# Kernel optimization log

Hardware: AMD Instinct MI355X
Metric: run time of the kernel (lower is better)

Reference implementation:

```python
import jax, jax.numpy as jnp
import numpy as np

GAMMA = 0.3      # LinearSpike surrogate slope (Bellec et al. 2018)
TIMESTEPS = 8
DROPOUT = 0.2

@jax.custom_vjp
def spike_fn(mem_thr):
    # forward: Heaviside spike; backward: piecewise-linear surrogate
    return (mem_thr > 0).astype(mem_thr.dtype)

def _spike_fwd(m):
    return (m > 0).astype(m.dtype), m

def _spike_bwd(m, g):
    return (GAMMA * jnp.maximum(1.0 - jnp.abs(m), 0.0) * g,)

spike_fn.defvjp(_spike_fwd, _spike_bwd)

def conv(x, w, stride=1, pad=1):
    return jax.lax.conv_general_dilated(
        x, w, (stride, stride), [(pad, pad), (pad, pad)],
        dimension_numbers=('NCHW', 'OIHW', 'NCHW'))

def avgpool2(x):
    B, C, H, W = x.shape
    return x.reshape(B, C, H // 2, 2, W // 2, 2).mean(axis=(3, 5))

def lif(mem, delta, leak, thr):
    mem = leak * mem + delta                  # leaky integrate
    mem_thr = mem / thr - 1.0                 # normalized membrane
    out = spike_fn(mem_thr)                   # binary spike
    mem = mem - thr * (mem_thr > 0).astype(mem.dtype)  # soft reset
    return mem, out

def setup_inputs() -> dict:
    key = jax.random.key(0)
    ks = jax.random.split(key, 24)
    B = 32
    def w(k, o, i, kh):
        std = float(np.sqrt(2.0 / (kh * kh * o)))  # matches _initialize_weights2
        return jax.random.normal(k, (o, i, kh, kh), jnp.float32) * std
    def mask(k, shape):
        keep = jax.random.bernoulli(k, 1.0 - DROPOUT, shape)
        return keep.astype(jnp.float32) / (1.0 - DROPOUT)
    return {
        'x': jax.random.normal(ks[0], (B, 3, 32, 32), jnp.float32),
        'w_pre0': w(ks[1], 64, 3, 3),
        'w_pre1': w(ks[2], 64, 64, 3),
        'w_pre2': w(ks[3], 64, 64, 3),
        'w1a': w(ks[4], 64, 64, 3),  'w1b': w(ks[5], 64, 64, 3),
        'w2a': w(ks[6], 128, 64, 3), 'w2b': w(ks[7], 128, 128, 3), 'w2i': w(ks[8], 128, 64, 1),
        'w3a': w(ks[9], 256, 128, 3), 'w3b': w(ks[10], 256, 256, 3), 'w3i': w(ks[11], 256, 128, 1),
        'w4a': w(ks[12], 512, 256, 3), 'w4b': w(ks[13], 512, 512, 3), 'w4i': w(ks[14], 512, 256, 1),
        'w_fc': jax.random.normal(ks[15], (10, 512 * 2 * 2), jnp.float32) * 0.01,
        'thr': jnp.ones((11,), jnp.float32),
        'leak': jnp.ones((11,), jnp.float32),
        'mask2': mask(ks[16], (B, 64, 32, 32)),
        'mask5': mask(ks[17], (B, 64, 32, 32)),
        'mask9': mask(ks[18], (B, 64, 16, 16)),
        'mask11': mask(ks[19], (B, 128, 8, 8)),
        'mask13': mask(ks[20], (B, 256, 4, 4)),
        'mask15': mask(ks[21], (B, 512, 2, 2)),
    }

def _forward(x, w_pre0, w_pre1, w_pre2, w1a, w1b, w2a, w2b, w2i,
             w3a, w3b, w3i, w4a, w4b, w4i, w_fc, thr, leak,
             mask2, mask5, mask9, mask11, mask13, mask15):
    B = x.shape[0]
    f32 = jnp.float32
    mems0 = (
        jnp.zeros((B, 64, 32, 32), f32), jnp.zeros((B, 64, 32, 32), f32),
        jnp.zeros((B, 64, 32, 32), f32),
        jnp.zeros((B, 64, 16, 16), f32), jnp.zeros((B, 64, 16, 16), f32),
        jnp.zeros((B, 128, 8, 8), f32), jnp.zeros((B, 128, 8, 8), f32),
        jnp.zeros((B, 256, 4, 4), f32), jnp.zeros((B, 256, 4, 4), f32),
        jnp.zeros((B, 512, 2, 2), f32), jnp.zeros((B, 512, 2, 2), f32),
        jnp.zeros((B, 10), f32),  # output accumulator mem
    )

    def step(carry, _):
        m0, m1, m2, m3, m4, m5, m6, m7, m8, m9, m10, mfc = carry
        # pre_process: (conv->spike->dropout) x2, conv->spike, avgpool2
        m0, o = lif(m0, conv(x, w_pre0), leak[0], thr[0]); o = o * mask2
        m1, o = lif(m1, conv(o, w_pre1), leak[1], thr[1]); o = o * mask5
        m2, o = lif(m2, conv(o, w_pre2), leak[2], thr[2])
        o = avgpool2(o)  # 32x32 -> 16x16
        # layer1 BasicBlock (stride 1, identity shortcut)
        inp = o
        m3, o = lif(m3, conv(inp, w1a), leak[3], thr[3]); o = o * mask9
        m4, o = lif(m4, conv(o, w1b) + inp, leak[4], thr[4])
        # layer2 BasicBlock (stride 2, 1x1 conv shortcut)
        inp = o
        m5, o = lif(m5, conv(inp, w2a, stride=2), leak[5], thr[5]); o = o * mask11
        m6, o = lif(m6, conv(o, w2b) + conv(inp, w2i, stride=2, pad=0), leak[6], thr[6])
        # layer3
        inp = o
        m7, o = lif(m7, conv(inp, w3a, stride=2), leak[7], thr[7]); o = o * mask13
        m8, o = lif(m8, conv(o, w3b) + conv(inp, w3i, stride=2, pad=0), leak[8], thr[8])
        # layer4
        inp = o
        m9, o = lif(m9, conv(inp, w4a, stride=2), leak[9], thr[9]); o = o * mask15
        m10, o = lif(m10, conv(o, w4b) + conv(inp, w4i, stride=2, pad=0), leak[10], thr[10])
        # output layer: pure accumulation of classifier current over timesteps
        mfc = mfc + o.reshape(B, -1) @ w_fc.T
        return (m0, m1, m2, m3, m4, m5, m6, m7, m8, m9, m10, mfc), None

    carry, _ = jax.lax.scan(step, mems0, None, length=TIMESTEPS)
    return carry[-1]  # [B, labels]

def reference(x, w_pre0, w_pre1, w_pre2, w1a, w1b, w2a, w2b, w2i,
              w3a, w3b, w3i, w4a, w4b, w4i, w_fc, thr, leak,
              mask2, mask5, mask9, mask11, mask13, mask15):
    return _forward(x, w_pre0, w_pre1, w_pre2, w1a, w1b, w2a, w2b, w2i,
                    w3a, w3b, w3i, w4a, w4b, w4i, w_fc, thr, leak,
                    mask2, mask5, mask9, mask11, mask13, mask15)
```

## Files before the change

### kernel.cpp

```cpp
#include <hip/hip_runtime.h>

#define BATCH 32

template<int H, int KS>
__global__ __launch_bounds__(256) void conv64_v2(
    const float* __restrict__ in, const float* __restrict__ w,
    float* __restrict__ pbuf)
{
    constexpr int W    = H;
    constexpr int QR   = W / 4;
    constexpr int ROWS = 64 / QR;
    constexpr int RS   = W + 4;
    constexpr int CC   = 8;
    constexpr int PLANE = (ROWS + 2) * RS;
    constexpr int CCT  = 64 / KS;
    constexpr int NCH  = CCT / CC;
    constexpr int NTOT = 32 * 64 * H * W;
    __shared__ float sIn[CC * PLANE];

    const int tid  = threadIdx.x;
    const int b    = blockIdx.x;
    const int rt   = blockIdx.y;
    const int zc   = blockIdx.z;
    const int cg   = zc & 1;
    const int ks   = zc >> 1;
    const int lane = tid & 63;
    const int g    = __builtin_amdgcn_readfirstlane(tid >> 6);
    const int octet = cg * 32 + g * 8;
    const int r    = lane / QR;
    const int wq   = lane % QR;
    const int ho   = rt * ROWS + r;
    const int row0 = rt * ROWS;

    float acc[8][4] = {};
    const size_t in_b = (size_t)b * 64 * H * W;

    for (int ch = 0; ch < NCH; ++ch) {
        const int c0 = ks * CCT + ch * CC;
        if (ch) __syncthreads();
        constexpr int LCNT = CC * (ROWS + 2) * (W + 2);
        for (int i = tid; i < LCNT; i += 256) {
            int c   = i / ((ROWS + 2) * (W + 2));
            int rr  = (i / (W + 2)) % (ROWS + 2);
            int col = i % (W + 2);
            int ih  = row0 + rr - 1;
            int iw  = col - 1;
            float v = 0.f;
            if ((unsigned)ih < (unsigned)H && (unsigned)iw < (unsigned)W)
                v = in[in_b + (size_t)(c0 + c) * H * W + ih * W + iw];
            sIn[c * PLANE + rr * RS + col] = v;
        }
        __syncthreads();

        for (int c = 0; c < CC; ++c) {
            float rv[3][6];
            #pragma unroll
            for (int dr = 0; dr < 3; ++dr) {
                const float* p = &sIn[c * PLANE + (r + dr) * RS + wq * 4];
                float4 a  = *(const float4*)p;
                float2 b2 = *(const float2*)(p + 4);
                rv[dr][0] = a.x;  rv[dr][1] = a.y; rv[dr][2] = a.z; rv[dr][3] = a.w;
                rv[dr][4] = b2.x; rv[dr][5] = b2.y;
            }
            const float* wc = w + ((size_t)octet * 64 + (c0 + c)) * 9;
            #pragma unroll
            for (int j = 0; j < 8; ++j) {
                const float* wk = wc + (size_t)j * 64 * 9;
                float w0 = wk[0], w1 = wk[1], w2 = wk[2];
                float w3 = wk[3], w4 = wk[4], w5 = wk[5];
                float w6 = wk[6], w7 = wk[7], w8 = wk[8];
                #pragma unroll
                for (int k = 0; k < 4; ++k) {
                    acc[j][k] = fmaf(rv[0][k + 0], w0, acc[j][k]);
                    acc[j][k] = fmaf(rv[0][k + 1], w1, acc[j][k]);
                    acc[j][k] = fmaf(rv[0][k + 2], w2, acc[j][k]);
                    acc[j][k] = fmaf(rv[1][k + 0], w3, acc[j][k]);
                    acc[j][k] = fmaf(rv[1][k + 1], w4, acc[j][k]);
                    acc[j][k] = fmaf(rv[1][k + 2], w5, acc[j][k]);
                    acc[j][k] = fmaf(rv[2][k + 0], w6, acc[j][k]);
                    acc[j][k] = fmaf(rv[2][k + 1], w7, acc[j][k]);
                    acc[j][k] = fmaf(rv[2][k + 2], w8, acc[j][k]);
                }
            }
        }
    }

    #pragma unroll
    for (int j = 0; j < 8; ++j) {
        const size_t idx = ((size_t)(b * 64 + octet + j) * H + ho) * W + wq * 4;
        *(float4*)&pbuf[(size_t)ks * NTOT + idx] =
            make_float4(acc[j][0], acc[j][1], acc[j][2], acc[j][3]);
    }
}

template<int KS>
__global__ __launch_bounds__(256) void conv_l2b(
    const float* __restrict__ in,
    const float* __restrict__ w,
    const float* __restrict__ sc_in,
    const float* __restrict__ sc_w,
    float* __restrict__ pbuf)
{
    constexpr int CI = 128, CO = 128, SC_CI = 64;
    constexpr int CC  = CI / KS;
    constexpr int SCC = SC_CI / KS;
    constexpr int BSTR = 52;
    constexpr int CST  = 32 * BSTR;
    constexpr int BSTRs = 36;
    constexpr int CSTs  = 32 * BSTRs;
    constexpr int NTOT = 32 * CO * 64;
    __shared__ float sBuf[CC * CST];

    const int tid  = threadIdx.x;
    const int lane = tid & 63;
    const int b    = lane >> 1;
    const int co_u = __builtin_amdgcn_readfirstlane(blockIdx.y * 4 + (tid >> 6));
    const int ks   = blockIdx.x;
    const int sp   = blockIdx.z;
    const int r0   = sp * 4;

    for (int i = tid; i < CC * 32 * 12; i += 256) {
        int f4  = i % 2;
        int row = (i / 2) % 6;
        int bb  = (i / 12) % 32;
        int c   = i / 384;
        int gr  = r0 - 1 + row;
        float4 v = make_float4(0.f, 0.f, 0.f, 0.f);
        if ((unsigned)gr < 8u)
            v = *(const float4*)&in[(((size_t)bb * CI + ks * CC + c) * 8 + gr) * 8 + f4 * 4];
        *(float4*)&sBuf[c * CST + bb * BSTR + row * 8 + f4 * 4] = v;
    }
    __syncthreads();

    float acc[32] = {};
    #pragma unroll 2
    for (int c = 0; c < CC; ++c) {
        const float* wk = w + ((size_t)co_u * CI + ks * CC + c) * 9;
        float wr[9];
        #pragma unroll
        for (int q = 0; q < 9; ++q) wr[q] = wk[q];
        float pl[48];
        #pragma unroll
        for (int k = 0; k < 12; ++k) {
            float4 v = *(const float4*)&sBuf[c * CST + b * BSTR + k * 4];
            pl[k * 4 + 0] = v.x; pl[k * 4 + 1] = v.y;
            pl[k * 4 + 2] = v.z; pl[k * 4 + 3] = v.w;
        }
        #pragma unroll
        for (int oh = 0; oh < 4; ++oh) {
            #pragma unroll
            for (int ow = 0; ow < 8; ++ow) {
                #pragma unroll
                for (int kh = 0; kh < 3; ++kh) {
                    #pragma unroll
                    for (int kw = 0; kw < 3; ++kw) {
                        const int iw = ow - 1 + kw;
                        if (iw < 0 || iw >= 8) continue;
                        acc[oh * 8 + ow] = fmaf(pl[(oh + kh) * 8 + iw],
                                                wr[kh * 3 + kw], acc[oh * 8 + ow]);
                    }
                }
            }
        }
    }
    __syncthreads();

    for (int i = tid; i < SCC * 32 * 16; i += 256) {
        int q   = i % 4;
        int row = (i / 4) % 4;
        int bb  = (i / 16) % 32;
        int c   = i / 512;
        float4 v = *(const float4*)&sc_in[
            (((size_t)bb * SC_CI + ks * SCC + c) * 16 + 2 * (r0 + row)) * 16 + q * 4];
        sBuf[c * CSTs + bb * BSTRs + row * 8 + q * 2 + 0] = v.x;
        sBuf[c * CSTs + bb * BSTRs + row * 8 + q * 2 + 1] = v.z;
    }
    __syncthreads();

    #pragma unroll
    for (int c = 0; c < SCC; ++c) {
        float sw = sc_w[(size_t)co_u * SC_CI + ks * SCC + c];
        #pragma unroll
        for (int p4 = 0; p4 < 8; ++p4) {
            float4 v = *(const float4*)&sBuf[c * CSTs + b * BSTRs + p4 * 4];
            acc[p4 * 4 + 0] = fmaf(v.x, sw, acc[p4 * 4 + 0]);
            acc[p4 * 4 + 1] = fmaf(v.y, sw, acc[p4 * 4 + 1]);
            acc[p4 * 4 + 2] = fmaf(v.z, sw, acc[p4 * 4 + 2]);
            acc[p4 * 4 + 3] = fmaf(v.w, sw, acc[p4 * 4 + 3]);
        }
    }

    if ((lane & 1) == 0) {
        #pragma unroll
        for (int oh = 0; oh < 4; ++oh) {
            const size_t idx = ((size_t)(b * CO + co_u) * 8 + r0 + oh) * 8;
            *(float4*)&pbuf[(size_t)ks * NTOT + idx]     =
                make_float4(acc[oh * 8 + 0], acc[oh * 8 + 1], acc[oh * 8 + 2], acc[oh * 8 + 3]);
            *(float4*)&pbuf[(size_t)ks * NTOT + idx + 4] =
                make_float4(acc[oh * 8 + 4], acc[oh * 8 + 5], acc[oh * 8 + 6], acc[oh * 8 + 7]);
        }
    }
}

template<int CI, int HIN, int STRIDE, int CO, int SC_CI, int SC_HIN,
         int CC, int NB, int NT>
__global__ __launch_bounds__(NT) void conv_cb(
    const float* __restrict__ in, const float* __restrict__ w,
    const float* __restrict__ sc_in, const float* __restrict__ sc_w,
    float* __restrict__ mem,
    const float* __restrict__ thr_a, const float* __restrict__ leak_a, int layer,
    const float* __restrict__ mask,
    float* __restrict__ out,
    float* __restrict__ accum)
{
    constexpr int HOUT = (STRIDE == 2) ? HIN / 2 : HIN;
    constexpr int P    = HOUT * HOUT;
    constexpr int PW   = HIN + 2;
    constexpr int PP   = PW * PW;
    constexpr int PSTR = PP + 1;
    constexpr int CSTR = NB * PSTR;
    constexpr int NPIX = HIN * HIN;
    constexpr int COB  = NT / 128;
    static_assert(NB * P == 128, "block must cover 128 n");

    constexpr int SINSZ4 = (CC * CSTR + 3) / 4;
    __shared__ float4 sIn4[SINSZ4];
    float* sIn = (float*)sIn4;

    const int tid  = threadIdx.x;
    const int lane = tid & 63;
    const int col  = tid >> 7;
    const int nh   = (tid >> 6) & 1;
    const int n    = nh * 64 + lane;
    const int b_l  = n / P;
    const int pos  = n % P;
    const int ho   = pos / HOUT;
    const int wo   = pos % HOUT;
    const int co_u = __builtin_amdgcn_readfirstlane(blockIdx.y * COB + col);
    const int b    = blockIdx.x * NB + b_l;

    for (int i = tid; i < SINSZ4; i += NT)
        sIn4[i] = make_float4(0.f, 0.f, 0.f, 0.f);

    const int lbase = b_l * PSTR + (ho * STRIDE) * PW + (wo * STRIDE);
    const float* wrow = w + (size_t)co_u * CI * 9;
    float a0 = 0.f, a1 = 0.f, a2 = 0.f;

    for (int c0 = 0; c0 < CI; c0 += CC) {
        __syncthreads();
        constexpr int NF4 = CC * NB * NPIX / 4;
        for (int i = tid; i < NF4; i += NT) {
            int e   = i * 4;
            int c   = e / (NB * NPIX);
            int r   = e % (NB * NPIX);
            int bl  = r / NPIX;
            int pix = r % NPIX;
            float4 v = *(const float4*)&in[
                ((size_t)(blockIdx.x * NB + bl) * CI + (c0 + c)) * NPIX + pix];
            float vv[4] = {v.x, v.y, v.z, v.w};
            #pragma unroll
            for (int q = 0; q < 4; ++q) {
                int p  = pix + q;
                int ih = p / HIN, iw = p % HIN;
                sIn[c * CSTR + bl * PSTR + (ih + 1) * PW + (iw + 1)] = vv[q];
            }
        }
        __syncthreads();

        const float* wc = wrow + (size_t)c0 * 9;
        #pragma unroll 4
        for (int c = 0; c < CC; ++c) {
            const float* pp = &sIn[c * CSTR + lbase];
            const float* wk = wc + c * 9;
            float w0 = wk[0], w1 = wk[1], w2 = wk[2];
            float w3 = wk[3], w4 = wk[4], w5 = wk[5];
            float w6 = wk[6], w7 = wk[7], w8 = wk[8];
            a0 = fmaf(pp[0],          w0, a0);
            a1 = fmaf(pp[1],          w1, a1);
            a2 = fmaf(pp[2],          w2, a2);
            a0 = fmaf(pp[PW],         w3, a0);
            a1 = fmaf(pp[PW + 1],     w4, a1);
            a2 = fmaf(pp[PW + 2],     w5, a2);
            a0 = fmaf(pp[2 * PW],     w6, a0);
            a1 = fmaf(pp[2 * PW + 1], w7, a1);
            a2 = fmaf(pp[2 * PW + 2], w8, a2);
        }
    }

    float acc = a0 + a1 + a2;

    if constexpr (SC_CI > 0) {
        const float* swrow = sc_w + (size_t)co_u * SC_CI;
        const size_t sbase = (size_t)b * SC_CI * SC_HIN * SC_HIN
                           + (2 * ho) * SC_HIN + 2 * wo;
        constexpr int SPL = SC_HIN * SC_HIN;
        float s0 = 0.f, s1 = 0.f;
        #pragma unroll 4
        for (int ci = 0; ci < SC_CI; ci += 2) {
            s0 = fmaf(sc_in[sbase + (size_t)ci * SPL],       swrow[ci],     s0);
            s1 = fmaf(sc_in[sbase + (size_t)(ci + 1) * SPL], swrow[ci + 1], s1);
        }
        acc += s0 + s1;
    }

    const float thr  = thr_a[layer];
    const float leak = leak_a[layer];
    const size_t idx = (size_t)(b * CO + co_u) * P + pos;
    float m   = fmaf(leak, mem[idx], acc);
    float mth = m / thr - 1.0f;
    float sp  = (mth > 0.f) ? 1.f : 0.f;
    mem[idx]  = m - thr * sp;
    float o = sp;
    if (mask) o *= mask[idx];
    out[idx] = o;
    if (accum) accum[idx] += o;
}

template<int CI, int HIN, int STRIDE, int CO, int SC_CI, int SC_HIN,
         int KS, int COB>
__global__ __launch_bounds__(COB * 64) void conv_ks(
    const float* __restrict__ in, const float* __restrict__ w,
    const float* __restrict__ sc_in, const float* __restrict__ sc_w,
    float* __restrict__ pbuf)
{
    constexpr int NT   = COB * 64;
    constexpr int HOUT = (STRIDE == 2) ? HIN / 2 : HIN;
    constexpr int P    = HOUT * HOUT;
    constexpr int NPIX = HIN * HIN;
    constexpr int CC   = CI / KS;
    constexpr int SCC  = (SC_CI > 0) ? SC_CI / KS : 0;
    constexpr int BSTR = NPIX + (((NPIX / 4) % 2 == 0) ? 4 : 0);
    constexpr int CST  = 32 * BSTR;
    constexpr int BSTRs = P + (((P / 4) % 2 == 0) ? 4 : 0);
    constexpr int CSTs  = 32 * BSTRs;
    static_assert(CI % KS == 0, "ks split");
    static_assert(NPIX % 4 == 0 && P % 4 == 0, "vector widths");

    __shared__ float sIn[CC * CST];
    __shared__ float sSc[(SCC > 0) ? SCC * CSTs : 1];

    const int tid  = threadIdx.x;
    const int lane = tid & 63;
    const int b    = lane >> 1;
    const int ks   = blockIdx.x;
    const int co_u = __builtin_amdgcn_readfirstlane(blockIdx.y * COB + (tid >> 6));
    const int cb   = ks * CC;

    constexpr int NF4 = CC * 32 * (NPIX / 4);
    for (int i = tid; i < NF4; i += NT) {
        int k4 = i % (NPIX / 4);
        int c  = (i / (NPIX / 4)) % CC;
        int bb = i / ((NPIX / 4) * CC);
        float4 v = *(const float4*)&in[((size_t)bb * CI + cb + c) * NPIX + k4 * 4];
        *(float4*)&sIn[c * CST + bb * BSTR + k4 * 4] = v;
    }
    if constexpr (SCC > 0) {
        constexpr int NH  = HOUT / 2;
        constexpr int NSC = SCC * 32 * HOUT * NH;
        for (int i = tid; i < NSC; i += NT) {
            int hc = i % NH;
            int r  = (i / NH) % HOUT;
            int c  = (i / (NH * HOUT)) % SCC;
            int bb = i / (NH * HOUT * SCC);
            float4 v = *(const float4*)&sc_in[
                ((size_t)(bb * SC_CI + ks * SCC + c) * SC_HIN + 2 * r) * SC_HIN
                + hc * 4];
            sSc[c * CSTs + bb * BSTRs + r * HOUT + hc * 2 + 0] = v.x;
            sSc[c * CSTs + bb * BSTRs + r * HOUT + hc * 2 + 1] = v.z;
        }
    }
    __syncthreads();

    float acc[P] = {};

    const float* wbase = w + ((size_t)co_u * CI + cb) * 9;
    #pragma unroll 4
    for (int j = 0; j < CC; ++j) {
        float wr[9];
        #pragma unroll
        for (int q = 0; q < 9; ++q) wr[q] = wbase[j * 9 + q];
        float plane[NPIX];
        #pragma unroll
        for (int r4 = 0; r4 < NPIX / 4; ++r4) {
            float4 v = *(const float4*)&sIn[j * CST + b * BSTR + r4 * 4];
            plane[r4 * 4 + 0] = v.x; plane[r4 * 4 + 1] = v.y;
            plane[r4 * 4 + 2] = v.z; plane[r4 * 4 + 3] = v.w;
        }
        #pragma unroll
        for (int ho = 0; ho < HOUT; ++ho) {
            #pragma unroll
            for (int wo = 0; wo < HOUT; ++wo) {
                #pragma unroll
                for (int kh = 0; kh < 3; ++kh) {
                    const int ih = ho * STRIDE - 1 + kh;
                    if (ih < 0 || ih >= HIN) continue;
                    #pragma unroll
                    for (int kw = 0; kw < 3; ++kw) {
                        const int iw = wo * STRIDE - 1 + kw;
                        if (iw < 0 || iw >= HIN) continue;
                        acc[ho * HOUT + wo] =
                            fmaf(plane[ih * HIN + iw], wr[kh * 3 + kw],
                                 acc[ho * HOUT + wo]);
                    }
                }
            }
        }
    }

    if constexpr (SCC > 0) {
        const float* swb = sc_w + (size_t)co_u * SC_CI + ks * SCC;
        #pragma unroll 4
        for (int j = 0; j < SCC; ++j) {
            float sw = swb[j];
            #pragma unroll
            for (int p4 = 0; p4 < P / 4; ++p4) {
                float4 v = *(const float4*)&sSc[j * CSTs + b * BSTRs + p4 * 4];
                acc[p4 * 4 + 0] = fmaf(v.x, sw, acc[p4 * 4 + 0]);
                acc[p4 * 4 + 1] = fmaf(v.y, sw, acc[p4 * 4 + 1]);
                acc[p4 * 4 + 2] = fmaf(v.z, sw, acc[p4 * 4 + 2]);
                acc[p4 * 4 + 3] = fmaf(v.w, sw, acc[p4 * 4 + 3]);
            }
        }
    }

    if ((lane & 1) == 0) {
        float* pp = pbuf + (((size_t)ks * 32 + b) * CO + co_u) * P;
        #pragma unroll
        for (int p4 = 0; p4 < P / 4; ++p4)
            *(float4*)&pp[p4 * 4] = make_float4(acc[p4 * 4], acc[p4 * 4 + 1],
                                                acc[p4 * 4 + 2], acc[p4 * 4 + 3]);
    }
}

template<int CO, int P, int KS>
__global__ __launch_bounds__(256) void reduce_lif(
    const float* __restrict__ pbuf,
    const float* __restrict__ res,
    float* __restrict__ mem,
    const float* __restrict__ thr_a, const float* __restrict__ leak_a, int layer,
    const float* __restrict__ mask, float* __restrict__ out,
    float* __restrict__ accum)
{
    constexpr int TOT4 = 32 * CO * P / 4;
    const int i4 = blockIdx.x * 256 + threadIdx.x;
    if (i4 >= TOT4) return;
    const float4* pb4 = (const float4*)pbuf;
    float4 s = pb4[i4];
    #pragma unroll 4
    for (int ks = 1; ks < KS; ++ks) {
        float4 v = pb4[(size_t)ks * TOT4 + i4];
        s.x += v.x; s.y += v.y; s.z += v.z; s.w += v.w;
    }
    const size_t idx = (size_t)i4 * 4;
    if (res) {
        float4 r4 = *(const float4*)&res[idx];
        s.x += r4.x; s.y += r4.y; s.z += r4.z; s.w += r4.w;
    }
    const float thr  = thr_a[layer];
    const float leak = leak_a[layer];
    float4 m4 = *(const float4*)&mem[idx];
    float4 k4 = mask ? *(const float4*)&mask[idx] : make_float4(1.f, 1.f, 1.f, 1.f);
    float4 mo, oo;
    float m0 = fmaf(leak, m4.x, s.x); float s0 = (m0 / thr - 1.0f > 0.f) ? 1.f : 0.f;
    mo.x = m0 - thr * s0; oo.x = s0 * k4.x;
    float m1 = fmaf(leak, m4.y, s.y); float s1 = (m1 / thr - 1.0f > 0.f) ? 1.f : 0.f;
    mo.y = m1 - thr * s1; oo.y = s1 * k4.y;
    float m2 = fmaf(leak, m4.z, s.z); float s2 = (m2 / thr - 1.0f > 0.f) ? 1.f : 0.f;
    mo.z = m2 - thr * s2; oo.z = s2 * k4.z;
    float m3 = fmaf(leak, m4.w, s.w); float s3 = (m3 / thr - 1.0f > 0.f) ? 1.f : 0.f;
    mo.w = m3 - thr * s3; oo.w = s3 * k4.w;
    *(float4*)&mem[idx] = mo;
    *(float4*)&out[idx] = oo;
    if (accum) {
        float4 a4 = *(const float4*)&accum[idx];
        a4.x += oo.x; a4.y += oo.y; a4.z += oo.z; a4.w += oo.w;
        *(float4*)&accum[idx] = a4;
    }
}

__global__ __launch_bounds__(256) void conv_raw_kernel(
    const float* __restrict__ in, const float* __restrict__ w,
    float* __restrict__ out,
    int Ci, int Co, int Hin, int Win, int total)
{
    int idx = blockIdx.x * blockDim.x + threadIdx.x;
    if (idx >= total) return;
    int wo = idx % Win;
    int t  = idx / Win;
    int ho = t % Hin; t /= Hin;
    int co = t % Co;
    int b  = t / Co;
    int ih0 = ho - 1, iw0 = wo - 1;
    const float* wp = w + (size_t)co * Ci * 9;
    const float* ip = in + (size_t)b * Ci * Hin * Win;
    bool hv0 = (unsigned)(ih0)     < (unsigned)Hin;
    bool hv1 = (unsigned)(ih0 + 1) < (unsigned)Hin;
    bool hv2 = (unsigned)(ih0 + 2) < (unsigned)Hin;
    bool wv0 = (unsigned)(iw0)     < (unsigned)Win;
    bool wv1 = (unsigned)(iw0 + 1) < (unsigned)Win;
    bool wv2 = (unsigned)(iw0 + 2) < (unsigned)Win;
    float acc = 0.f;
    int plane = Hin * Win;
    for (int ci = 0; ci < Ci; ++ci) {
        const float* irow = ip + ci * plane;
        const float* wk   = wp + ci * 9;
        if (hv0) {
            const float* r = irow + ih0 * Win;
            if (wv0) acc = fmaf(r[iw0],     wk[0], acc);
            if (wv1) acc = fmaf(r[iw0 + 1], wk[1], acc);
            if (wv2) acc = fmaf(r[iw0 + 2], wk[2], acc);
        }
        if (hv1) {
            const float* r = irow + (ih0 + 1) * Win;
            if (wv0) acc = fmaf(r[iw0],     wk[3], acc);
            if (wv1) acc = fmaf(r[iw0 + 1], wk[4], acc);
            if (wv2) acc = fmaf(r[iw0 + 2], wk[5], acc);
        }
        if (hv2) {
            const float* r = irow + (ih0 + 2) * Win;
            if (wv0) acc = fmaf(r[iw0],     wk[6], acc);
            if (wv1) acc = fmaf(r[iw0 + 1], wk[7], acc);
            if (wv2) acc = fmaf(r[iw0 + 2], wk[8], acc);
        }
    }
    out[idx] = acc;
}

__global__ __launch_bounds__(256) void lif0_kernel(
    const float4* __restrict__ delta, float4* __restrict__ mem,
    const float* __restrict__ thr_a, const float* __restrict__ leak_a,
    const float4* __restrict__ mask, float4* __restrict__ out, int total4)
{
    int i = blockIdx.x * blockDim.x + threadIdx.x;
    if (i >= total4) return;
    float thr = thr_a[0], leak = leak_a[0];
    float4 d = delta[i], m4 = mem[i], k4 = mask[i], mo, oo;
    float m0 = fmaf(leak, m4.x, d.x); float s0 = (m0 / thr - 1.0f > 0.f) ? 1.f : 0.f;
    mo.x = m0 - thr * s0; oo.x = s0 * k4.x;
    float m1 = fmaf(leak, m4.y, d.y); float s1 = (m1 / thr - 1.0f > 0.f) ? 1.f : 0.f;
    mo.y = m1 - thr * s1; oo.y = s1 * k4.y;
    float m2 = fmaf(leak, m4.z, d.z); float s2 = (m2 / thr - 1.0f > 0.f) ? 1.f : 0.f;
    mo.z = m2 - thr * s2; oo.z = s2 * k4.z;
    float m3 = fmaf(leak, m4.w, d.w); float s3 = (m3 / thr - 1.0f > 0.f) ? 1.f : 0.f;
    mo.w = m3 - thr * s3; oo.w = s3 * k4.w;
    mem[i] = mo; out[i] = oo;
}

__global__ __launch_bounds__(256) void avgpool_kernel(
    const float* __restrict__ in, float* __restrict__ out,
    int C, int Hout, int Wout, int total)
{
    int idx = blockIdx.x * blockDim.x + threadIdx.x;
    if (idx >= total) return;
    int wo = idx % Wout;
    int t  = idx / Wout;
    int ho = t % Hout; t /= Hout;
    int c  = t % C;
    int b  = t / C;
    int Hin = Hout * 2, Win = Wout * 2;
    const float* p = in + (((size_t)b * C + c) * Hin + 2 * ho) * Win + 2 * wo;
    out[idx] = (p[0] + p[1] + p[Win] + p[Win + 1]) * 0.25f;
}

__global__ __launch_bounds__(64) void fc_kernel(
    const float* __restrict__ s, const float* __restrict__ wfc,
    float* __restrict__ out)
{
    int bk = blockIdx.x;
    int b = bk / 10, k = bk % 10;
    const float* sp = s   + (size_t)b * 2048;
    const float* wp = wfc + (size_t)k * 2048;
    float acc = 0.f;
    for (int j = threadIdx.x; j < 2048; j += 64)
        acc = fmaf(sp[j], wp[j], acc);
    #pragma unroll
    for (int off = 32; off; off >>= 1)
        acc += __shfl_down(acc, off, 64);
    if (threadIdx.x == 0) out[b * 10 + k] = acc;
}

extern "C" void kernel_launch(void* const* d_in, const int* in_sizes, int n_in,
                              void* d_out, int out_size, void* d_ws, size_t ws_size,
                              hipStream_t stream) {
    const float* x      = (const float*)d_in[0];
    const float* w_pre0 = (const float*)d_in[1];
    const float* w_pre1 = (const float*)d_in[2];
    const float* w_pre2 = (const float*)d_in[3];
    const float* w1a    = (const float*)d_in[4];
    const float* w1b    = (const float*)d_in[5];
    const float* w2a    = (const float*)d_in[6];
    const float* w2b    = (const float*)d_in[7];
    const float* w2i    = (const float*)d_in[8];
    const float* w3a    = (const float*)d_in[9];
    const float* w3b    = (const float*)d_in[10];
    const float* w3i    = (const float*)d_in[11];
    const float* w4a    = (const float*)d_in[12];
    const float* w4b    = (const float*)d_in[13];
    const float* w4i    = (const float*)d_in[14];
    const float* w_fc   = (const float*)d_in[15];
    const float* thr    = (const float*)d_in[16];
    const float* leak   = (const float*)d_in[17];
    const float* mask2  = (const float*)d_in[18];
    const float* mask5  = (const float*)d_in[19];
    const float* mask9  = (const float*)d_in[20];
    const float* mask11 = (const float*)d_in[21];
    const float* mask13 = (const float*)d_in[22];
    const float* mask15 = (const float*)d_in[23];

    float* ws = (float*)d_ws;
    size_t off = 0;
    auto alloc = [&](size_t n) { float* p = ws + off; off += n; return p; };
    float* m0  = alloc(2097152);
    float* m1  = alloc(2097152);
    float* m2  = alloc(2097152);
    float* m3  = alloc(524288);
    float* m4  = alloc(524288);
    float* m5  = alloc(262144);
    float* m6  = alloc(262144);
    float* m7  = alloc(131072);
    float* m8  = alloc(131072);
    float* m9  = alloc(65536);
    float* m10 = alloc(65536);
    float* ssum = alloc(65536);
    size_t zero_floats = off;
    float* delta0  = alloc(2097152);
    float* s32_a   = alloc(2097152);
    float* s32_b   = alloc(2097152);
    float* s16_inp = alloc(524288);
    float* s16_a   = alloc(524288);
    float* s16_b   = alloc(524288);
    float* s8_a    = alloc(262144);
    float* s8_b    = alloc(262144);
    float* s4_a    = alloc(131072);
    float* s4_b    = alloc(131072);
    float* s2_a    = alloc(65536);
    float* s2_b    = alloc(65536);
    float* pbuf    = alloc(4194304);
    (void)ws_size; (void)in_sizes; (void)n_in; (void)out_size;

    hipMemsetAsync(d_ws, 0, zero_floats * sizeof(float), stream);

    auto grid = [](int total) { return dim3((total + 255) / 256); };

    {
        int total = BATCH * 64 * 32 * 32;
        conv_raw_kernel<<<grid(total), 256, 0, stream>>>(
            x, w_pre0, delta0, 3, 64, 32, 32, total);
    }

    for (int t = 0; t < 8; ++t) {
        int n32 = BATCH * 64 * 32 * 32;
        lif0_kernel<<<grid(n32 / 4), 256, 0, stream>>>(
            (const float4*)delta0, (float4*)m0, thr, leak,
            (const float4*)mask2, (float4*)s32_a, n32 / 4);
        conv64_v2<32, 2><<<dim3(BATCH, 4, 4), 256, 0, stream>>>(s32_a, w_pre1, pbuf);
        reduce_lif<64, 1024, 2><<<dim3(2048), 256, 0, stream>>>(
            pbuf, nullptr, m1, thr, leak, 1, mask5, s32_b, nullptr);
        conv64_v2<32, 2><<<dim3(BATCH, 4, 4), 256, 0, stream>>>(s32_b, w_pre2, pbuf);
        reduce_lif<64, 1024, 2><<<dim3(2048), 256, 0, stream>>>(
            pbuf, nullptr, m2, thr, leak, 2, nullptr, s32_a, nullptr);
        int n16 = BATCH * 64 * 16 * 16;
        avgpool_kernel<<<grid(n16), 256, 0, stream>>>(s32_a, s16_inp, 64, 16, 16, n16);
        conv64_v2<16, 4><<<dim3(BATCH, 1, 8), 256, 0, stream>>>(s16_inp, w1a, pbuf);
        reduce_lif<64, 256, 4><<<dim3(512), 256, 0, stream>>>(
            pbuf, nullptr, m3, thr, leak, 3, mask9, s16_a, nullptr);
        conv64_v2<16, 4><<<dim3(BATCH, 1, 8), 256, 0, stream>>>(s16_a, w1b, pbuf);
        reduce_lif<64, 256, 4><<<dim3(512), 256, 0, stream>>>(
            pbuf, s16_inp, m4, thr, leak, 4, nullptr, s16_b, nullptr);

        conv_cb<64, 16, 2, 128, 0, 0, 8, 2, 256><<<dim3(16, 64), 256, 0, stream>>>(
            s16_b, w2a, nullptr, nullptr, m5, thr, leak, 5, mask11, s8_a, nullptr);
        conv_l2b<16><<<dim3(16, 32, 2), 256, 0, stream>>>(
            s8_a, w2b, s16_b, w2i, pbuf);
        reduce_lif<128, 64, 16><<<dim3(256), 256, 0, stream>>>(
            pbuf, nullptr, m6, thr, leak, 6, nullptr, s8_b, nullptr);
        conv_ks<128, 8, 2, 256, 0, 0, 32, 4><<<dim3(32, 64), 256, 0, stream>>>(
            s8_b, w3a, nullptr, nullptr, pbuf);
        reduce_lif<256, 16, 32><<<dim3(128), 256, 0, stream>>>(
            pbuf, nullptr, m7, thr, leak, 7, mask13, s4_a, nullptr);
        conv_ks<256, 4, 1, 256, 128, 8, 16, 4><<<dim3(16, 64), 256, 0, stream>>>(
            s4_a, w3b, s8_b, w3i, pbuf);
        reduce_lif<256, 16, 16><<<dim3(128), 256, 0, stream>>>(
            pbuf, nullptr, m8, thr, leak, 8, nullptr, s4_b, nullptr);
        conv_ks<256, 4, 2, 512, 0, 0, 16, 4><<<dim3(16, 128), 256, 0, stream>>>(
            s4_b, w4a, nullptr, nullptr, pbuf);
        reduce_lif<512, 4, 16><<<dim3(64), 256, 0, stream>>>(
            pbuf, nullptr, m9, thr, leak, 9, mask15, s2_a, nullptr);
        conv_ks<512, 2, 1, 512, 256, 4, 16, 4><<<dim3(16, 128), 256, 0, stream>>>(
            s2_a, w4b, s4_b, w4i, pbuf);
        reduce_lif<512, 4, 16><<<dim3(64), 256, 0, stream>>>(
            pbuf, nullptr, m10, thr, leak, 10, nullptr, s2_b, ssum);
    }

    fc_kernel<<<dim3(320), dim3(64), 0, stream>>>(ssum, w_fc, (float*)d_out);
}
```

Measured before the change: 3.087 ms.

## Replace fused layer2a conv with split-K conv_mid and raise split-K elsewhere

```diff
diff --git a/kernel.cpp b/kernel.cpp
--- a/kernel.cpp
+++ b/kernel.cpp
@@ -93,6 +93,86 @@
     }
 }
 
+template<int CI, int CO, int KS, int RT>
+__global__ __launch_bounds__(256) void conv_mid(
+    const float* __restrict__ in,
+    const float* __restrict__ w,
+    float* __restrict__ pbuf)
+{
+    constexpr int HIN = 16, HOUT = 8;
+    constexpr int CC  = CI / KS;
+    constexpr int NR  = (RT - 1) * 2 + 3;
+    constexpr int BSTR = NR * HIN + 4;
+    constexpr int CST  = 32 * BSTR;
+    constexpr int NTOT = 32 * CO * HOUT * HOUT;
+    __shared__ float sBuf[CC * CST];
+
+    const int tid  = threadIdx.x;
+    const int lane = tid & 63;
+    const int b    = lane >> 1;
+    const int ks   = blockIdx.x;
+    const int co_u = __builtin_amdgcn_readfirstlane(blockIdx.y * 4 + (tid >> 6));
+    const int r0   = blockIdx.z * RT;
+    const int g0   = r0 * 2 - 1;
+
+    for (int i = tid; i < CC * 32 * NR * 4; i += 256) {
+        int q  = i % 4;
+        int s  = (i / 4) % NR;
+        int bb = (i / (4 * NR)) % 32;
+        int c  = i / (4 * NR * 32);
+        int gr = g0 + s;
+        float4 v = make_float4(0.f, 0.f, 0.f, 0.f);
+        if ((unsigned)gr < (unsigned)HIN)
+            v = *(const float4*)&in[(((size_t)bb * CI + ks * CC + c) * HIN + gr) * HIN + q * 4];
+        *(float4*)&sBuf[c * CST + bb * BSTR + s * HIN + q * 4] = v;
+    }
+    __syncthreads();
+
+    float acc[RT * 8] = {};
+    #pragma unroll 2
+    for (int c = 0; c < CC; ++c) {
+        const float* wk = w + ((size_t)co_u * CI + ks * CC + c) * 9;
+        float wr[9];
+        #pragma unroll
+        for (int q = 0; q < 9; ++q) wr[q] = wk[q];
+        float pl[NR * HIN];
+        #pragma unroll
+        for (int k = 0; k < NR * 4; ++k) {
+            float4 v = *(const float4*)&sBuf[c * CST + b * BSTR + k * 4];
+            pl[k * 4 + 0] = v.x; pl[k * 4 + 1] = v.y;
+            pl[k * 4 + 2] = v.z; pl[k * 4 + 3] = v.w;
+        }
+        #pragma unroll
+        for (int j = 0; j < RT; ++j) {
+            #pragma unroll
+            for (int ow = 0; ow < 8; ++ow) {
+                #pragma unroll
+                for (int kh = 0; kh < 3; ++kh) {
+                    const int s = 2 * j + kh;
+                    #pragma unroll
+                    for (int kw = 0; kw < 3; ++kw) {
+                        const int iw = 2 * ow - 1 + kw;
+                        if (iw < 0 || iw >= HIN) continue;
+                        acc[j * 8 + ow] = fmaf(pl[s * HIN + iw], wr[kh * 3 + kw],
+                                               acc[j * 8 + ow]);
+                    }
+                }
+            }
+        }
+    }
+
+    if ((lane & 1) == 0) {
+        #pragma unroll
+        for (int j = 0; j < RT; ++j) {
+            const size_t idx = ((size_t)(b * CO + co_u) * HOUT + r0 + j) * HOUT;
+            *(float4*)&pbuf[(size_t)ks * NTOT + idx]     =
+                make_float4(acc[j * 8 + 0], acc[j * 8 + 1], acc[j * 8 + 2], acc[j * 8 + 3]);
+            *(float4*)&pbuf[(size_t)ks * NTOT + idx + 4] =
+                make_float4(acc[j * 8 + 4], acc[j * 8 + 5], acc[j * 8 + 6], acc[j * 8 + 7]);
+        }
+    }
+}
+
 template<int KS>
 __global__ __launch_bounds__(256) void conv_l2b(
     const float* __restrict__ in,
@@ -200,120 +280,6 @@
                 make_float4(acc[oh * 8 + 4], acc[oh * 8 + 5], acc[oh * 8 + 6], acc[oh * 8 + 7]);
         }
     }
-}
-
-template<int CI, int HIN, int STRIDE, int CO, int SC_CI, int SC_HIN,
-         int CC, int NB, int NT>
-__global__ __launch_bounds__(NT) void conv_cb(
-    const float* __restrict__ in, const float* __restrict__ w,
-    const float* __restrict__ sc_in, const float* __restrict__ sc_w,
-    float* __restrict__ mem,
-    const float* __restrict__ thr_a, const float* __restrict__ leak_a, int layer,
-    const float* __restrict__ mask,
-    float* __restrict__ out,
-    float* __restrict__ accum)
-{
-    constexpr int HOUT = (STRIDE == 2) ? HIN / 2 : HIN;
-    constexpr int P    = HOUT * HOUT;
-    constexpr int PW   = HIN + 2;
-    constexpr int PP   = PW * PW;
-    constexpr int PSTR = PP + 1;
-    constexpr int CSTR = NB * PSTR;
-    constexpr int NPIX = HIN * HIN;
-    constexpr int COB  = NT / 128;
-    static_assert(NB * P == 128, "block must cover 128 n");
-
-    constexpr int SINSZ4 = (CC * CSTR + 3) / 4;
-    __shared__ float4 sIn4[SINSZ4];
-    float* sIn = (float*)sIn4;
-
-    const int tid  = threadIdx.x;
-    const int lane = tid & 63;
-    const int col  = tid >> 7;
-    const int nh   = (tid >> 6) & 1;
-    const int n    = nh * 64 + lane;
-    const int b_l  = n / P;
-    const int pos  = n % P;
-    const int ho   = pos / HOUT;
-    const int wo   = pos % HOUT;
-    const int co_u = __builtin_amdgcn_readfirstlane(blockIdx.y * COB + col);
-    const int b    = blockIdx.x * NB + b_l;
-
-    for (int i = tid; i < SINSZ4; i += NT)
-        sIn4[i] = make_float4(0.f, 0.f, 0.f, 0.f);
-
-    const int lbase = b_l * PSTR + (ho * STRIDE) * PW + (wo * STRIDE);
-    const float* wrow = w + (size_t)co_u * CI * 9;
-    float a0 = 0.f, a1 = 0.f, a2 = 0.f;
-
-    for (int c0 = 0; c0 < CI; c0 += CC) {
-        __syncthreads();
-        constexpr int NF4 = CC * NB * NPIX / 4;
-        for (int i = tid; i < NF4; i += NT) {
-            int e   = i * 4;
-            int c   = e / (NB * NPIX);
-            int r   = e % (NB * NPIX);
-            int bl  = r / NPIX;
-            int pix = r % NPIX;
-            float4 v = *(const float4*)&in[
-                ((size_t)(blockIdx.x * NB + bl) * CI + (c0 + c)) * NPIX + pix];
-            float vv[4] = {v.x, v.y, v.z, v.w};
-            #pragma unroll
-            for (int q = 0; q < 4; ++q) {
-                int p  = pix + q;
-                int ih = p / HIN, iw = p % HIN;
-                sIn[c * CSTR + bl * PSTR + (ih + 1) * PW + (iw + 1)] = vv[q];
-            }
-        }
-        __syncthreads();
-
-        const float* wc = wrow + (size_t)c0 * 9;
-        #pragma unroll 4
-        for (int c = 0; c < CC; ++c) {
-            const float* pp = &sIn[c * CSTR + lbase];
-            const float* wk = wc + c * 9;
-            float w0 = wk[0], w1 = wk[1], w2 = wk[2];
-            float w3 = wk[3], w4 = wk[4], w5 = wk[5];
-            float w6 = wk[6], w7 = wk[7], w8 = wk[8];
-            a0 = fmaf(pp[0],          w0, a0);
-            a1 = fmaf(pp[1],          w1, a1);
-            a2 = fmaf(pp[2],          w2, a2);
-            a0 = fmaf(pp[PW],         w3, a0);
-            a1 = fmaf(pp[PW + 1],     w4, a1);
-            a2 = fmaf(pp[PW + 2],     w5, a2);
-            a0 = fmaf(pp[2 * PW],     w6, a0);
-            a1 = fmaf(pp[2 * PW + 1], w7, a1);
-            a2 = fmaf(pp[2 * PW + 2], w8, a2);
-        }
-    }
-
-    float acc = a0 + a1 + a2;
-
-    if constexpr (SC_CI > 0) {
-        const float* swrow = sc_w + (size_t)co_u * SC_CI;
-        const size_t sbase = (size_t)b * SC_CI * SC_HIN * SC_HIN
-                           + (2 * ho) * SC_HIN + 2 * wo;
-        constexpr int SPL = SC_HIN * SC_HIN;
-        float s0 = 0.f, s1 = 0.f;
-        #pragma unroll 4
-        for (int ci = 0; ci < SC_CI; ci += 2) {
-            s0 = fmaf(sc_in[sbase + (size_t)ci * SPL],       swrow[ci],     s0);
-            s1 = fmaf(sc_in[sbase + (size_t)(ci + 1) * SPL], swrow[ci + 1], s1);
-        }
-        acc += s0 + s1;
-    }
-
-    const float thr  = thr_a[layer];
-    const float leak = leak_a[layer];
-    const size_t idx = (size_t)(b * CO + co_u) * P + pos;
-    float m   = fmaf(leak, mem[idx], acc);
-    float mth = m / thr - 1.0f;
-    float sp  = (mth > 0.f) ? 1.f : 0.f;
-    mem[idx]  = m - thr * sp;
-    float o = sp;
-    if (mask) o *= mask[idx];
-    out[idx] = o;
-    if (accum) accum[idx] += o;
 }
 
 template<int CI, int HIN, int STRIDE, int CO, int SC_CI, int SC_HIN,
@@ -635,7 +601,7 @@
     float* s4_b    = alloc(131072);
     float* s2_a    = alloc(65536);
     float* s2_b    = alloc(65536);
-    float* pbuf    = alloc(4194304);
+    float* pbuf    = alloc(8388608);
     (void)ws_size; (void)in_sizes; (void)n_in; (void)out_size;
 
     hipMemsetAsync(d_ws, 0, zero_floats * sizeof(float), stream);
@@ -653,23 +619,25 @@
         lif0_kernel<<<grid(n32 / 4), 256, 0, stream>>>(
             (const float4*)delta0, (float4*)m0, thr, leak,
             (const float4*)mask2, (float4*)s32_a, n32 / 4);
-        conv64_v2<32, 2><<<dim3(BATCH, 4, 4), 256, 0, stream>>>(s32_a, w_pre1, pbuf);
-        reduce_lif<64, 1024, 2><<<dim3(2048), 256, 0, stream>>>(
+        conv64_v2<32, 4><<<dim3(BATCH, 4, 8), 256, 0, stream>>>(s32_a, w_pre1, pbuf);
+        reduce_lif<64, 1024, 4><<<dim3(2048), 256, 0, stream>>>(
             pbuf, nullptr, m1, thr, leak, 1, mask5, s32_b, nullptr);
-        conv64_v2<32, 2><<<dim3(BATCH, 4, 4), 256, 0, stream>>>(s32_b, w_pre2, pbuf);
-        reduce_lif<64, 1024, 2><<<dim3(2048), 256, 0, stream>>>(
+        conv64_v2<32, 4><<<dim3(BATCH, 4, 8), 256, 0, stream>>>(s32_b, w_pre2, pbuf);
+        reduce_lif<64, 1024, 4><<<dim3(2048), 256, 0, stream>>>(
             pbuf, nullptr, m2, thr, leak, 2, nullptr, s32_a, nullptr);
         int n16 = BATCH * 64 * 16 * 16;
         avgpool_kernel<<<grid(n16), 256, 0, stream>>>(s32_a, s16_inp, 64, 16, 16, n16);
-        conv64_v2<16, 4><<<dim3(BATCH, 1, 8), 256, 0, stream>>>(s16_inp, w1a, pbuf);
-        reduce_lif<64, 256, 4><<<dim3(512), 256, 0, stream>>>(
+        conv64_v2<16, 8><<<dim3(BATCH, 1, 16), 256, 0, stream>>>(s16_inp, w1a, pbuf);
+        reduce_lif<64, 256, 8><<<dim3(512), 256, 0, stream>>>(
             pbuf, nullptr, m3, thr, leak, 3, mask9, s16_a, nullptr);
-        conv64_v2<16, 4><<<dim3(BATCH, 1, 8), 256, 0, stream>>>(s16_a, w1b, pbuf);
-        reduce_lif<64, 256, 4><<<dim3(512), 256, 0, stream>>>(
+        conv64_v2<16, 8><<<dim3(BATCH, 1, 16), 256, 0, stream>>>(s16_a, w1b, pbuf);
+        reduce_lif<64, 256, 8><<<dim3(512), 256, 0, stream>>>(
             pbuf, s16_inp, m4, thr, leak, 4, nullptr, s16_b, nullptr);
 
-        conv_cb<64, 16, 2, 128, 0, 0, 8, 2, 256><<<dim3(16, 64), 256, 0, stream>>>(
-            s16_b, w2a, nullptr, nullptr, m5, thr, leak, 5, mask11, s8_a, nullptr);
+        conv_mid<64, 128, 16, 2><<<dim3(16, 32, 4), 256, 0, stream>>>(
+            s16_b, w2a, pbuf);
+        reduce_lif<128, 64, 16><<<dim3(256), 256, 0, stream>>>(
+            pbuf, nullptr, m5, thr, leak, 5, mask11, s8_a, nullptr);
         conv_l2b<16><<<dim3(16, 32, 2), 256, 0, stream>>>(
             s8_a, w2b, s16_b, w2i, pbuf);
         reduce_lif<128, 64, 16><<<dim3(256), 256, 0, stream>>>(
```

Result: faster. 2.850 ms (-7.7%).
